# Optimization experiments

Hardware: AMD Instinct MI355X
Metric: run time of the kernel (lower is better)

## Reference

```python
import jax, jax.numpy as jnp
from jax import lax
import numpy as np

DIM = 64
NUM_HEADS = 1
HEAD_DIM = DIM // NUM_HEADS
SR = 8
EPS = 1e-5


def setup_inputs() -> dict:
    key = jax.random.key(0)
    ks = jax.random.split(key, 12)
    B, H, W = 8, 128, 128
    N = H * W
    s = 1.0 / np.sqrt(DIM)
    x = jax.random.normal(ks[0], (B, N, DIM), dtype=jnp.float32)
    Wq = jax.random.normal(ks[1], (DIM, DIM), dtype=jnp.float32) * s
    bq = jnp.zeros((DIM,), jnp.float32)
    Wk = jax.random.normal(ks[2], (DIM, DIM), dtype=jnp.float32) * s
    bk = jnp.zeros((DIM,), jnp.float32)
    Wv = jax.random.normal(ks[3], (DIM, DIM), dtype=jnp.float32) * s
    bv = jnp.zeros((DIM,), jnp.float32)
    # Conv2D kernel in HWIO layout (Keras default), kernel=stride=SR, padding VALID
    Wsr = jax.random.normal(ks[4], (SR, SR, DIM, DIM), dtype=jnp.float32) * (1.0 / np.sqrt(SR * SR * DIM))
    bsr = jnp.zeros((DIM,), jnp.float32)
    gamma = jnp.ones((DIM,), jnp.float32)
    beta = jnp.zeros((DIM,), jnp.float32)
    Wp = jax.random.normal(ks[5], (DIM, DIM), dtype=jnp.float32) * s
    bp = jnp.zeros((DIM,), jnp.float32)
    return {"x": x, "Wq": Wq, "bq": bq, "Wk": Wk, "bk": bk, "Wv": Wv, "bv": bv,
            "Wsr": Wsr, "bsr": bsr, "gamma": gamma, "beta": beta, "Wp": Wp, "bp": bp,
            "H": H, "W": W}


def reference(x, Wq, bq, Wk, bk, Wv, bv, Wsr, bsr, gamma, beta, Wp, bp, H, W):
    B, N, C = x.shape
    # queries: [B, heads, N, head_dim]
    q = (x @ Wq + bq).reshape(B, N, NUM_HEADS, HEAD_DIM).transpose(0, 2, 1, 3)
    # spatial reduction: strided conv over the token grid, then LayerNorm
    xs = x.reshape(B, H, W, C)
    xs = lax.conv_general_dilated(xs, Wsr, window_strides=(SR, SR), padding='VALID',
                                  dimension_numbers=('NHWC', 'HWIO', 'NHWC')) + bsr
    xs = xs.reshape(B, -1, C)  # [B, Nkv, C], Nkv = (H//SR)*(W//SR)
    mu = jnp.mean(xs, axis=-1, keepdims=True)
    var = jnp.var(xs, axis=-1, keepdims=True)
    xs = (xs - mu) * lax.rsqrt(var + EPS) * gamma + beta
    k = (xs @ Wk + bk).reshape(B, -1, NUM_HEADS, HEAD_DIM).transpose(0, 2, 1, 3)
    v = (xs @ Wv + bv).reshape(B, -1, NUM_HEADS, HEAD_DIM).transpose(0, 2, 1, 3)
    scale = jnp.asarray(np.sqrt(HEAD_DIM), x.dtype)
    attn = jnp.einsum('bhqd,bhkd->bhqk', q, k) / scale
    attn = jax.nn.softmax(attn, axis=-1)
    out = jnp.einsum('bhqk,bhkd->bhqd', attn, v)
    out = out.transpose(0, 2, 1, 3).reshape(B, N, NUM_HEADS * HEAD_DIM)
    return out @ Wp + bp
```

## Files before the change

kernel.cpp:

```cpp
#include <hip/hip_runtime.h>

typedef unsigned short u16;
typedef short short8 __attribute__((ext_vector_type(8)));
typedef short short4v __attribute__((ext_vector_type(4)));
typedef float f32x4 __attribute__((ext_vector_type(4)));
typedef float f4 __attribute__((ext_vector_type(4)));

#define MFMA16(a, b, c) __builtin_amdgcn_mfma_f32_16x16x32_bf16(a, b, c, 0, 0, 0)
#define MFMA1K(a, b, c) __builtin_amdgcn_mfma_f32_16x16x16bf16_1k(a, b, c, 0, 0, 0)

__device__ inline u16 f2bf(float f) {
    unsigned int v = __builtin_bit_cast(unsigned int, f);
    unsigned int r = (v + 0x7FFFu + ((v >> 16) & 1u)) >> 16;
    return (u16)r;
}
__device__ inline short4v pack4(f4 v) {
    short4v r;
#pragma unroll
    for (int j = 0; j < 4; ++j) r[j] = (short)f2bf(v[j]);
    return r;
}

__global__ __launch_bounds__(256) void prep_kernel(
    const float* __restrict__ Wsr, const float* __restrict__ Wq,
    const float* __restrict__ Wp,
    u16* __restrict__ WsrT, u16* __restrict__ WqT, u16* __restrict__ WpT)
{
    const int bid = blockIdx.x;
    const int tid = threadIdx.x;
    __shared__ float sT[64 * 65];
    const float* src;
    u16* dst;
    if (bid < 64)      { src = Wsr + (size_t)bid * 4096; dst = WsrT + (size_t)bid * 4096; }
    else if (bid == 64){ src = Wq;  dst = WqT; }
    else               { src = Wp;  dst = WpT; }
#pragma unroll
    for (int p = 0; p < 4; ++p) {
        int idx = p * 256 + tid;
        int r = idx >> 4, c4 = (idx & 15) * 4;
        f4 v = *(const f4*)(src + r * 64 + c4);
#pragma unroll
        for (int j = 0; j < 4; ++j) sT[r * 65 + c4 + j] = v[j];
    }
    __syncthreads();
#pragma unroll
    for (int p = 0; p < 2; ++p) {
        int idx = p * 256 + tid;
        int co = idx >> 3, g = (idx & 7) * 8;
        short8 o;
#pragma unroll
        for (int j = 0; j < 8; ++j) o[j] = (short)f2bf(sT[(g + j) * 65 + co]);
        *(short8*)(dst + (size_t)co * 64 + g) = o;
    }
}

__global__ __launch_bounds__(256) void conv_partial_kernel(
    const float* __restrict__ x, const u16* __restrict__ WsrT,
    float* __restrict__ partials)
{
    const int mtile  = blockIdx.x & 31;
    const int ksplit = blockIdx.x >> 5;
    const int tid  = threadIdx.x;
    const int wave = tid >> 6;
    const int lane = tid & 63;
    const int l15  = lane & 15;
    const int quad = lane >> 4;

    __shared__ u16 sA[64 * 72];
    __shared__ u16 sB[64 * 72];

    f32x4 acc[4];
#pragma unroll
    for (int nt = 0; nt < 4; ++nt) { acc[nt][0]=0.f; acc[nt][1]=0.f; acc[nt][2]=0.f; acc[nt][3]=0.f; }

    const int token0 = mtile * 64;
    for (int chunk = 0; chunk < 4; ++chunk) {
        const int cell = ksplit * 4 + chunk;
        const int py = cell >> 3, px = cell & 7;
        __syncthreads();
#pragma unroll
        for (int p = 0; p < 4; ++p) {
            int idx = p * 256 + tid;
            int r = idx >> 4, c4 = (idx & 15) * 4;
            int token = token0 + r;
            int b = token >> 8, rm = token & 255;
            int oy = rm >> 4, ox = rm & 15;
            int y = oy * 8 + py, xc = ox * 8 + px;
            f4 xv = *(const f4*)(x + ((size_t)(b * 16384 + y * 128 + xc)) * 64 + c4);
            short4v s;
#pragma unroll
            for (int j = 0; j < 4; ++j) s[j] = (short)f2bf(xv[j]);
            *(short4v*)&sA[r * 72 + c4] = s;
        }
#pragma unroll
        for (int p = 0; p < 2; ++p) {
            int idx = p * 256 + tid;
            int co = idx >> 3, g = (idx & 7) * 8;
            *(short8*)&sB[co * 72 + g] =
                *(const short8*)(WsrT + (size_t)cell * 4096 + co * 64 + g);
        }
        __syncthreads();
#pragma unroll
        for (int ks = 0; ks < 2; ++ks) {
            short8 af = *(const short8*)&sA[(wave * 16 + l15) * 72 + ks * 32 + quad * 8];
#pragma unroll
            for (int nt = 0; nt < 4; ++nt) {
                short8 bf = *(const short8*)&sB[(nt * 16 + l15) * 72 + ks * 32 + quad * 8];
                acc[nt] = MFMA16(af, bf, acc[nt]);
            }
        }
    }
    float* outp = partials + (size_t)ksplit * 131072;
#pragma unroll
    for (int nt = 0; nt < 4; ++nt)
#pragma unroll
        for (int i = 0; i < 4; ++i) {
            int row = token0 + wave * 16 + quad * 4 + i;
            outp[(size_t)row * 64 + nt * 16 + l15] = acc[nt][i];
        }
}

__global__ __launch_bounds__(256) void lnkv_kernel(
    const float* __restrict__ partials, const float* __restrict__ bsr,
    const float* __restrict__ gamma, const float* __restrict__ beta,
    const float* __restrict__ Wk, const float* __restrict__ bk,
    const float* __restrict__ Wv, const float* __restrict__ bv,
    u16* __restrict__ kbuf, u16* __restrict__ vTbuf)
{
    const int wave = threadIdx.x >> 6;
    const int c    = threadIdx.x & 63;
    const int token = blockIdx.x * 4 + wave;

    float acc = 0.f;
#pragma unroll
    for (int s = 0; s < 16; ++s)
        acc += partials[(size_t)s * 131072 + (size_t)token * 64 + c];
    acc += bsr[c];

    float sum = acc, sumsq = acc * acc;
#pragma unroll
    for (int m = 1; m < 64; m <<= 1) {
        sum   += __shfl_xor(sum, m, 64);
        sumsq += __shfl_xor(sumsq, m, 64);
    }
    float mean = sum * (1.f / 64.f);
    float var  = sumsq * (1.f / 64.f) - mean * mean;
    float inv  = rsqrtf(var + 1e-5f);
    float xn   = (acc - mean) * inv * gamma[c] + beta[c];

    __shared__ float sxn[4][64];
    sxn[wave][c] = xn;

    float ka = bk[c], va = bv[c];
#pragma unroll 8
    for (int ci = 0; ci < 64; ++ci) {
        float xv = sxn[wave][ci];
        ka += xv * Wk[ci * 64 + c];
        va += xv * Wv[ci * 64 + c];
    }
    kbuf[(size_t)token * 64 + c] = f2bf(ka);
    int b = token >> 8, t = token & 255;
    vTbuf[(size_t)b * 16384 + c * 256 + t] = f2bf(va);
}

__global__ __launch_bounds__(512) void attn_kernel(
    const float* __restrict__ x, const u16* __restrict__ WqT,
    const float* __restrict__ bq, const u16* __restrict__ WpT,
    const float* __restrict__ bp, const u16* __restrict__ kbuf,
    const u16* __restrict__ vTbuf, float* __restrict__ out)
{
    const int batch = blockIdx.x >> 6;
    const int row0  = (blockIdx.x & 63) * 256;
    const int tid  = threadIdx.x;
    const int wave = tid >> 6;
    const int lane = tid & 63;
    const int l15  = lane & 15;
    const int quad = lane >> 4;

    __shared__ u16 sK[256 * 72];
    __shared__ u16 sV[64 * 264];
    __shared__ u16 sWq[64 * 72];
    __shared__ u16 sWp[64 * 72];

#pragma unroll
    for (int p = 0; p < 4; ++p) {
        int idx = p * 512 + tid; int tt = idx >> 3, seg = idx & 7;
        *(short8*)&sK[tt * 72 + seg * 8] =
            *(const short8*)(kbuf + ((size_t)(batch * 256 + tt)) * 64 + seg * 8);
    }
#pragma unroll
    for (int p = 0; p < 4; ++p) {
        int idx = p * 512 + tid; int d = idx >> 5, seg = idx & 31;
        *(short8*)&sV[d * 264 + seg * 8] =
            *(const short8*)(vTbuf + ((size_t)(batch * 64 + d)) * 256 + seg * 8);
    }
    {
        int co = tid >> 3, g = (tid & 7) * 8;
        *(short8*)&sWq[co * 72 + g] = *(const short8*)(WqT + (size_t)co * 64 + g);
        *(short8*)&sWp[co * 72 + g] = *(const short8*)(WpT + (size_t)co * 64 + g);
    }
    __syncthreads();

    const int qbase = row0 + wave * 32;

    f32x4 qT[2][4];
#pragma unroll
    for (int qt = 0; qt < 2; ++qt)
#pragma unroll
        for (int ct = 0; ct < 4; ++ct) { qT[qt][ct][0]=0.f; qT[qt][ct][1]=0.f; qT[qt][ct][2]=0.f; qT[qt][ct][3]=0.f; }
#pragma unroll
    for (int kt = 0; kt < 4; ++kt) {
        short4v bfr[2];
#pragma unroll
        for (int qt = 0; qt < 2; ++qt) {
            f4 xv = *(const f4*)(x + ((size_t)(batch * 16384 + qbase + qt * 16 + l15)) * 64 + kt * 16 + quad * 4);
            bfr[qt] = pack4(xv);
        }
#pragma unroll
        for (int ct = 0; ct < 4; ++ct) {
            short4v a = *(const short4v*)&sWq[(ct * 16 + l15) * 72 + kt * 16 + quad * 4];
#pragma unroll
            for (int qt = 0; qt < 2; ++qt) qT[qt][ct] = MFMA1K(a, bfr[qt], qT[qt][ct]);
        }
    }
    short4v qf[2][4];
#pragma unroll
    for (int ct = 0; ct < 4; ++ct) {
        f4 bqv = *(const f4*)(bq + ct * 16 + quad * 4);
#pragma unroll
        for (int qt = 0; qt < 2; ++qt) {
            f4 t;
#pragma unroll
            for (int i = 0; i < 4; ++i) t[i] = (qT[qt][ct][i] + bqv[i]) * 0.125f;
            qf[qt][ct] = pack4(t);
        }
    }

    f32x4 st[2][16];
#pragma unroll
    for (int qt = 0; qt < 2; ++qt)
#pragma unroll
        for (int mt = 0; mt < 16; ++mt) { st[qt][mt][0]=0.f; st[qt][mt][1]=0.f; st[qt][mt][2]=0.f; st[qt][mt][3]=0.f; }
#pragma unroll
    for (int mt = 0; mt < 16; ++mt)
#pragma unroll
        for (int kt = 0; kt < 4; ++kt) {
            short4v a = *(const short4v*)&sK[(mt * 16 + l15) * 72 + kt * 16 + quad * 4];
#pragma unroll
            for (int qt = 0; qt < 2; ++qt) st[qt][mt] = MFMA1K(a, qf[qt][kt], st[qt][mt]);
        }

    short4v pf[2][16];
    float linv[2];
#pragma unroll
    for (int qt = 0; qt < 2; ++qt) {
        float mx = -1e30f;
#pragma unroll
        for (int mt = 0; mt < 16; ++mt)
#pragma unroll
            for (int i = 0; i < 4; ++i) mx = fmaxf(mx, st[qt][mt][i]);
        mx = fmaxf(mx, __shfl_xor(mx, 16, 64));
        mx = fmaxf(mx, __shfl_xor(mx, 32, 64));
        float l = 0.f;
#pragma unroll
        for (int mt = 0; mt < 16; ++mt) {
            f4 e;
#pragma unroll
            for (int i = 0; i < 4; ++i) { e[i] = __expf(st[qt][mt][i] - mx); l += e[i]; }
            pf[qt][mt] = pack4(e);
        }
        l += __shfl_xor(l, 16, 64);
        l += __shfl_xor(l, 32, 64);
        linv[qt] = 1.0f / l;
    }

    f32x4 ot[2][4];
#pragma unroll
    for (int qt = 0; qt < 2; ++qt)
#pragma unroll
        for (int dt = 0; dt < 4; ++dt) { ot[qt][dt][0]=0.f; ot[qt][dt][1]=0.f; ot[qt][dt][2]=0.f; ot[qt][dt][3]=0.f; }
#pragma unroll
    for (int mt = 0; mt < 16; ++mt)
#pragma unroll
        for (int dt = 0; dt < 4; ++dt) {
            short4v a = *(const short4v*)&sV[(dt * 16 + l15) * 264 + mt * 16 + quad * 4];
#pragma unroll
            for (int qt = 0; qt < 2; ++qt) ot[qt][dt] = MFMA1K(a, pf[qt][mt], ot[qt][dt]);
        }

    short4v of[2][4];
#pragma unroll
    for (int dt = 0; dt < 4; ++dt)
#pragma unroll
        for (int qt = 0; qt < 2; ++qt) {
            f4 t;
#pragma unroll
            for (int i = 0; i < 4; ++i) t[i] = ot[qt][dt][i] * linv[qt];
            of[qt][dt] = pack4(t);
        }
    f32x4 ft[2][4];
#pragma unroll
    for (int qt = 0; qt < 2; ++qt)
#pragma unroll
        for (int ct = 0; ct < 4; ++ct) { ft[qt][ct][0]=0.f; ft[qt][ct][1]=0.f; ft[qt][ct][2]=0.f; ft[qt][ct][3]=0.f; }
#pragma unroll
    for (int kt = 0; kt < 4; ++kt)
#pragma unroll
        for (int ct = 0; ct < 4; ++ct) {
            short4v a = *(const short4v*)&sWp[(ct * 16 + l15) * 72 + kt * 16 + quad * 4];
#pragma unroll
            for (int qt = 0; qt < 2; ++qt) ft[qt][ct] = MFMA1K(a, of[qt][kt], ft[qt][ct]);
        }

#pragma unroll
    for (int ct = 0; ct < 4; ++ct) {
        f4 bpv = *(const f4*)(bp + ct * 16 + quad * 4);
#pragma unroll
        for (int qt = 0; qt < 2; ++qt) {
            f4 r;
#pragma unroll
            for (int i = 0; i < 4; ++i) r[i] = ft[qt][ct][i] + bpv[i];
            *(f4*)(out + ((size_t)(batch * 16384 + qbase + qt * 16 + l15)) * 64 + ct * 16 + quad * 4) = r;
        }
    }
}

extern "C" void kernel_launch(void* const* d_in, const int* in_sizes, int n_in,
                              void* d_out, int out_size, void* d_ws, size_t ws_size,
                              hipStream_t stream) {
    const float* x     = (const float*)d_in[0];
    const float* Wq    = (const float*)d_in[1];
    const float* bq    = (const float*)d_in[2];
    const float* Wk    = (const float*)d_in[3];
    const float* bk    = (const float*)d_in[4];
    const float* Wv    = (const float*)d_in[5];
    const float* bv    = (const float*)d_in[6];
    const float* Wsr   = (const float*)d_in[7];
    const float* bsr   = (const float*)d_in[8];
    const float* gamma = (const float*)d_in[9];
    const float* beta  = (const float*)d_in[10];
    const float* Wp    = (const float*)d_in[11];
    const float* bp    = (const float*)d_in[12];

    char* w = (char*)d_ws;
    float* partials = (float*)w;
    u16* kbuf  = (u16*)(w + 8388608);
    u16* vTbuf = (u16*)(w + 8388608 + 262144);
    u16* WsrT  = (u16*)(w + 8388608 + 524288);
    u16* WqT   = (u16*)(w + 8388608 + 524288 + 524288);
    u16* WpT   = (u16*)(w + 8388608 + 524288 + 524288 + 8192);
    float* out = (float*)d_out;

    prep_kernel<<<66, 256, 0, stream>>>(Wsr, Wq, Wp, WsrT, WqT, WpT);
    conv_partial_kernel<<<512, 256, 0, stream>>>(x, WsrT, partials);
    lnkv_kernel<<<512, 256, 0, stream>>>(partials, bsr, gamma, beta, Wk, bk, Wv, bv, kbuf, vTbuf);
    attn_kernel<<<512, 512, 0, stream>>>(x, WqT, bq, WpT, bp, kbuf, vTbuf, out);
}
```

Before: 143.9 us.

## Fuse strided conv with LayerNorm and K/V projection, prefetch x in attention

Merges the split-K conv partial kernel and the LayerNorm+KV kernel into one kernel. Each block handles 8 tokens, and each wave accumulates 16 of the 64 kernel cells through MFMA reading directly from global memory. Partial sums are reduced in shared memory, which removes the 8 MB partials buffer round-trip and one launch. Half the MFMA rows are wasted, since only 8 tokens are padded into 16-row tiles, and only 256 blocks launch. The attention kernel also issues its x loads before the K/V shared-memory fill to hide their latency.

```diff
diff --git a/kernel.cpp b/kernel.cpp
--- a/kernel.cpp
+++ b/kernel.cpp
@@ -54,113 +54,91 @@
     }
 }
 
-__global__ __launch_bounds__(256) void conv_partial_kernel(
+__global__ __launch_bounds__(256) void convlnkv_kernel(
     const float* __restrict__ x, const u16* __restrict__ WsrT,
-    float* __restrict__ partials)
+    const float* __restrict__ bsr,
+    const float* __restrict__ gamma, const float* __restrict__ beta,
+    const float* __restrict__ Wk, const float* __restrict__ bk,
+    const float* __restrict__ Wv, const float* __restrict__ bv,
+    u16* __restrict__ kbuf, u16* __restrict__ vTbuf)
 {
-    const int mtile  = blockIdx.x & 31;
-    const int ksplit = blockIdx.x >> 5;
     const int tid  = threadIdx.x;
     const int wave = tid >> 6;
     const int lane = tid & 63;
     const int l15  = lane & 15;
     const int quad = lane >> 4;
 
-    __shared__ u16 sA[64 * 72];
-    __shared__ u16 sB[64 * 72];
+    const int t0   = blockIdx.x * 8;
+    const int bimg = t0 >> 8;
+    const int rm0  = t0 & 255;
+    const int oy   = rm0 >> 4;
+    const int ox   = (rm0 & 15) + (l15 & 7);
 
     f32x4 acc[4];
 #pragma unroll
     for (int nt = 0; nt < 4; ++nt) { acc[nt][0]=0.f; acc[nt][1]=0.f; acc[nt][2]=0.f; acc[nt][3]=0.f; }
 
-    const int token0 = mtile * 64;
-    for (int chunk = 0; chunk < 4; ++chunk) {
-        const int cell = ksplit * 4 + chunk;
+#pragma unroll
+    for (int i = 0; i < 16; ++i) {
+        const int cell = wave * 16 + i;
         const int py = cell >> 3, px = cell & 7;
-        __syncthreads();
-#pragma unroll
-        for (int p = 0; p < 4; ++p) {
-            int idx = p * 256 + tid;
-            int r = idx >> 4, c4 = (idx & 15) * 4;
-            int token = token0 + r;
-            int b = token >> 8, rm = token & 255;
-            int oy = rm >> 4, ox = rm & 15;
-            int y = oy * 8 + py, xc = ox * 8 + px;
-            f4 xv = *(const f4*)(x + ((size_t)(b * 16384 + y * 128 + xc)) * 64 + c4);
-            short4v s;
-#pragma unroll
-            for (int j = 0; j < 4; ++j) s[j] = (short)f2bf(xv[j]);
-            *(short4v*)&sA[r * 72 + c4] = s;
-        }
-#pragma unroll
-        for (int p = 0; p < 2; ++p) {
-            int idx = p * 256 + tid;
-            int co = idx >> 3, g = (idx & 7) * 8;
-            *(short8*)&sB[co * 72 + g] =
-                *(const short8*)(WsrT + (size_t)cell * 4096 + co * 64 + g);
-        }
-        __syncthreads();
+        const float* xp = x + ((size_t)(bimg * 16384 + (oy * 8 + py) * 128 + ox * 8 + px)) * 64;
+        const u16*   wp = WsrT + (size_t)cell * 4096;
 #pragma unroll
         for (int ks = 0; ks < 2; ++ks) {
-            short8 af = *(const short8*)&sA[(wave * 16 + l15) * 72 + ks * 32 + quad * 8];
+            f4 x0 = *(const f4*)(xp + ks * 32 + quad * 8);
+            f4 x1 = *(const f4*)(xp + ks * 32 + quad * 8 + 4);
+            short8 af;
+#pragma unroll
+            for (int j = 0; j < 4; ++j) { af[j] = (short)f2bf(x0[j]); af[4 + j] = (short)f2bf(x1[j]); }
 #pragma unroll
             for (int nt = 0; nt < 4; ++nt) {
-                short8 bf = *(const short8*)&sB[(nt * 16 + l15) * 72 + ks * 32 + quad * 8];
+                short8 bf = *(const short8*)(wp + (nt * 16 + l15) * 64 + ks * 32 + quad * 8);
                 acc[nt] = MFMA16(af, bf, acc[nt]);
             }
         }
     }
-    float* outp = partials + (size_t)ksplit * 131072;
-#pragma unroll
-    for (int nt = 0; nt < 4; ++nt)
-#pragma unroll
-        for (int i = 0; i < 4; ++i) {
-            int row = token0 + wave * 16 + quad * 4 + i;
-            outp[(size_t)row * 64 + nt * 16 + l15] = acc[nt][i];
-        }
-}
-
-__global__ __launch_bounds__(256) void lnkv_kernel(
-    const float* __restrict__ partials, const float* __restrict__ bsr,
-    const float* __restrict__ gamma, const float* __restrict__ beta,
-    const float* __restrict__ Wk, const float* __restrict__ bk,
-    const float* __restrict__ Wv, const float* __restrict__ bv,
-    u16* __restrict__ kbuf, u16* __restrict__ vTbuf)
-{
-    const int wave = threadIdx.x >> 6;
-    const int c    = threadIdx.x & 63;
-    const int token = blockIdx.x * 4 + wave;
-
-    float acc = 0.f;
-#pragma unroll
-    for (int s = 0; s < 16; ++s)
-        acc += partials[(size_t)s * 131072 + (size_t)token * 64 + c];
-    acc += bsr[c];
-
-    float sum = acc, sumsq = acc * acc;
-#pragma unroll
-    for (int m = 1; m < 64; m <<= 1) {
-        sum   += __shfl_xor(sum, m, 64);
-        sumsq += __shfl_xor(sumsq, m, 64);
-    }
-    float mean = sum * (1.f / 64.f);
-    float var  = sumsq * (1.f / 64.f) - mean * mean;
-    float inv  = rsqrtf(var + 1e-5f);
-    float xn   = (acc - mean) * inv * gamma[c] + beta[c];
-
-    __shared__ float sxn[4][64];
-    sxn[wave][c] = xn;
-
-    float ka = bk[c], va = bv[c];
+
+    __shared__ float red[4][8][64];
+    if (quad < 2) {
+#pragma unroll
+        for (int nt = 0; nt < 4; ++nt)
+#pragma unroll
+            for (int i = 0; i < 4; ++i)
+                red[wave][quad * 4 + i][nt * 16 + l15] = acc[nt][i];
+    }
+    __syncthreads();
+
+    __shared__ float sxn[8][64];
+#pragma unroll
+    for (int s = 0; s < 2; ++s) {
+        const int tt    = wave * 2 + s;
+        const int token = t0 + tt;
+        const int c     = lane;
+        float a = red[0][tt][c] + red[1][tt][c] + red[2][tt][c] + red[3][tt][c] + bsr[c];
+        float sum = a, sumsq = a * a;
+#pragma unroll
+        for (int m = 1; m < 64; m <<= 1) {
+            sum   += __shfl_xor(sum, m, 64);
+            sumsq += __shfl_xor(sumsq, m, 64);
+        }
+        float mean = sum * (1.f / 64.f);
+        float var  = sumsq * (1.f / 64.f) - mean * mean;
+        float inv  = rsqrtf(var + 1e-5f);
+        float xn   = (a - mean) * inv * gamma[c] + beta[c];
+        sxn[tt][c] = xn;
+
+        float ka = bk[c], va = bv[c];
 #pragma unroll 8
-    for (int ci = 0; ci < 64; ++ci) {
-        float xv = sxn[wave][ci];
-        ka += xv * Wk[ci * 64 + c];
-        va += xv * Wv[ci * 64 + c];
-    }
-    kbuf[(size_t)token * 64 + c] = f2bf(ka);
-    int b = token >> 8, t = token & 255;
-    vTbuf[(size_t)b * 16384 + c * 256 + t] = f2bf(va);
+        for (int ci = 0; ci < 64; ++ci) {
+            float xv = sxn[tt][ci];
+            ka += xv * Wk[ci * 64 + c];
+            va += xv * Wv[ci * 64 + c];
+        }
+        kbuf[(size_t)token * 64 + c] = f2bf(ka);
+        int bb = token >> 8, tloc = token & 255;
+        vTbuf[(size_t)bb * 16384 + c * 256 + tloc] = f2bf(va);
+    }
 }
 
 __global__ __launch_bounds__(512) void attn_kernel(
@@ -182,6 +160,15 @@
     __shared__ u16 sWq[64 * 72];
     __shared__ u16 sWp[64 * 72];
 
+    const int qbase = row0 + wave * 32;
+
+    f4 xq[4][2];
+#pragma unroll
+    for (int kt = 0; kt < 4; ++kt)
+#pragma unroll
+        for (int qt = 0; qt < 2; ++qt)
+            xq[kt][qt] = *(const f4*)(x + ((size_t)(batch * 16384 + qbase + qt * 16 + l15)) * 64 + kt * 16 + quad * 4);
+
 #pragma unroll
     for (int p = 0; p < 4; ++p) {
         int idx = p * 512 + tid; int tt = idx >> 3, seg = idx & 7;
@@ -201,8 +188,6 @@
     }
     __syncthreads();
 
-    const int qbase = row0 + wave * 32;
-
     f32x4 qT[2][4];
 #pragma unroll
     for (int qt = 0; qt < 2; ++qt)
@@ -212,10 +197,7 @@
     for (int kt = 0; kt < 4; ++kt) {
         short4v bfr[2];
 #pragma unroll
-        for (int qt = 0; qt < 2; ++qt) {
-            f4 xv = *(const f4*)(x + ((size_t)(batch * 16384 + qbase + qt * 16 + l15)) * 64 + kt * 16 + quad * 4);
-            bfr[qt] = pack4(xv);
-        }
+        for (int qt = 0; qt < 2; ++qt) bfr[qt] = pack4(xq[kt][qt]);
 #pragma unroll
         for (int ct = 0; ct < 4; ++ct) {
             short4v a = *(const short4v*)&sWq[(ct * 16 + l15) * 72 + kt * 16 + quad * 4];
@@ -343,16 +325,14 @@
     const float* bp    = (const float*)d_in[12];
 
     char* w = (char*)d_ws;
-    float* partials = (float*)w;
-    u16* kbuf  = (u16*)(w + 8388608);
-    u16* vTbuf = (u16*)(w + 8388608 + 262144);
-    u16* WsrT  = (u16*)(w + 8388608 + 524288);
-    u16* WqT   = (u16*)(w + 8388608 + 524288 + 524288);
-    u16* WpT   = (u16*)(w + 8388608 + 524288 + 524288 + 8192);
+    u16* kbuf  = (u16*)w;
+    u16* vTbuf = (u16*)(w + 262144);
+    u16* WsrT  = (u16*)(w + 524288);
+    u16* WqT   = (u16*)(w + 1048576);
+    u16* WpT   = (u16*)(w + 1048576 + 8192);
     float* out = (float*)d_out;
 
     prep_kernel<<<66, 256, 0, stream>>>(Wsr, Wq, Wp, WsrT, WqT, WpT);
-    conv_partial_kernel<<<512, 256, 0, stream>>>(x, WsrT, partials);
-    lnkv_kernel<<<512, 256, 0, stream>>>(partials, bsr, gamma, beta, Wk, bk, Wv, bv, kbuf, vTbuf);
+    convlnkv_kernel<<<256, 256, 0, stream>>>(x, WsrT, bsr, gamma, beta, Wk, bk, Wv, bv, kbuf, vTbuf);
     attn_kernel<<<512, 512, 0, stream>>>(x, WqT, bq, WpT, bp, kbuf, vTbuf, out);
 }
```

Result: slower. 156.5 us (+8.8%).

## Load conv operands directly from global into MFMA fragments; prefetch x in attention

Applied to the files above, without the earlier changes.

The conv partial kernel no longer stages the x tile and Wsr tile through shared memory. Each lane now loads its MFMA A fragment straight from global x, converts it to bf16, and reads B fragments directly from global WsrT, and the chunk loop is fully unrolled. This removes the shared-memory writes and two barriers per chunk, at the cost of less coalesced global loads and the same weight fragments being re-read from L1/L2 by every wave. In the attention kernel, the x rows for the Q projection are now issued into registers before the K/V/W shared-memory staging, so their latency overlaps that work, which raises register pressure.

```diff
diff --git a/kernel.cpp b/kernel.cpp
--- a/kernel.cpp
+++ b/kernel.cpp
@@ -66,46 +66,32 @@
     const int l15  = lane & 15;
     const int quad = lane >> 4;
 
-    __shared__ u16 sA[64 * 72];
-    __shared__ u16 sB[64 * 72];
-
     f32x4 acc[4];
 #pragma unroll
     for (int nt = 0; nt < 4; ++nt) { acc[nt][0]=0.f; acc[nt][1]=0.f; acc[nt][2]=0.f; acc[nt][3]=0.f; }
 
     const int token0 = mtile * 64;
+    const int token = token0 + wave * 16 + l15;
+    const int b  = token >> 8, rm = token & 255;
+    const int oy = rm >> 4,    ox = rm & 15;
+    const float* xbase = x + ((size_t)(b * 16384 + (oy * 8) * 128 + ox * 8)) * 64;
+
+#pragma unroll
     for (int chunk = 0; chunk < 4; ++chunk) {
         const int cell = ksplit * 4 + chunk;
         const int py = cell >> 3, px = cell & 7;
-        __syncthreads();
-#pragma unroll
-        for (int p = 0; p < 4; ++p) {
-            int idx = p * 256 + tid;
-            int r = idx >> 4, c4 = (idx & 15) * 4;
-            int token = token0 + r;
-            int b = token >> 8, rm = token & 255;
-            int oy = rm >> 4, ox = rm & 15;
-            int y = oy * 8 + py, xc = ox * 8 + px;
-            f4 xv = *(const f4*)(x + ((size_t)(b * 16384 + y * 128 + xc)) * 64 + c4);
-            short4v s;
-#pragma unroll
-            for (int j = 0; j < 4; ++j) s[j] = (short)f2bf(xv[j]);
-            *(short4v*)&sA[r * 72 + c4] = s;
-        }
-#pragma unroll
-        for (int p = 0; p < 2; ++p) {
-            int idx = p * 256 + tid;
-            int co = idx >> 3, g = (idx & 7) * 8;
-            *(short8*)&sB[co * 72 + g] =
-                *(const short8*)(WsrT + (size_t)cell * 4096 + co * 64 + g);
-        }
-        __syncthreads();
+        const float* xp = xbase + ((size_t)(py * 128 + px)) * 64;
+        const u16*   wp = WsrT + (size_t)cell * 4096;
 #pragma unroll
         for (int ks = 0; ks < 2; ++ks) {
-            short8 af = *(const short8*)&sA[(wave * 16 + l15) * 72 + ks * 32 + quad * 8];
+            f4 x0 = *(const f4*)(xp + ks * 32 + quad * 8);
+            f4 x1 = *(const f4*)(xp + ks * 32 + quad * 8 + 4);
+            short8 af;
+#pragma unroll
+            for (int j = 0; j < 4; ++j) { af[j] = (short)f2bf(x0[j]); af[4 + j] = (short)f2bf(x1[j]); }
 #pragma unroll
             for (int nt = 0; nt < 4; ++nt) {
-                short8 bf = *(const short8*)&sB[(nt * 16 + l15) * 72 + ks * 32 + quad * 8];
+                short8 bf = *(const short8*)(wp + (nt * 16 + l15) * 64 + ks * 32 + quad * 8);
                 acc[nt] = MFMA16(af, bf, acc[nt]);
             }
         }
@@ -182,6 +168,15 @@
     __shared__ u16 sWq[64 * 72];
     __shared__ u16 sWp[64 * 72];
 
+    const int qbase = row0 + wave * 32;
+
+    f4 xq[4][2];
+#pragma unroll
+    for (int kt = 0; kt < 4; ++kt)
+#pragma unroll
+        for (int qt = 0; qt < 2; ++qt)
+            xq[kt][qt] = *(const f4*)(x + ((size_t)(batch * 16384 + qbase + qt * 16 + l15)) * 64 + kt * 16 + quad * 4);
+
 #pragma unroll
     for (int p = 0; p < 4; ++p) {
         int idx = p * 512 + tid; int tt = idx >> 3, seg = idx & 7;
@@ -201,8 +196,6 @@
     }
     __syncthreads();
 
-    const int qbase = row0 + wave * 32;
-
     f32x4 qT[2][4];
 #pragma unroll
     for (int qt = 0; qt < 2; ++qt)
@@ -212,10 +205,7 @@
     for (int kt = 0; kt < 4; ++kt) {
         short4v bfr[2];
 #pragma unroll
-        for (int qt = 0; qt < 2; ++qt) {
-            f4 xv = *(const f4*)(x + ((size_t)(batch * 16384 + qbase + qt * 16 + l15)) * 64 + kt * 16 + quad * 4);
-            bfr[qt] = pack4(xv);
-        }
+        for (int qt = 0; qt < 2; ++qt) bfr[qt] = pack4(xq[kt][qt]);
 #pragma unroll
         for (int ct = 0; ct < 4; ++ct) {
             short4v a = *(const short4v*)&sWq[(ct * 16 + l15) * 72 + kt * 16 + quad * 4];
```

Result: slower. 150.3 us (+4.5%).

## Process query tiles sequentially to cut registers and raise attention occupancy

Applied to the files above, without the earlier changes.

The attention kernel now handles its two 16-row query tiles one after another in a loop instead of interleaved, which roughly halves the live accumulator and probability registers. Launch bounds request 4 blocks per CU. The Wq/Wp weights are read straight from global memory (cache) instead of being staged in LDS, which frees LDS and removes that staging step. The first tile's x rows are prefetched before the K/V LDS fill to overlap that load. The cost is less MFMA interleaving between independent tiles and repeated global weight reads per wave.

```diff
diff --git a/kernel.cpp b/kernel.cpp
--- a/kernel.cpp
+++ b/kernel.cpp
@@ -163,7 +163,7 @@
     vTbuf[(size_t)b * 16384 + c * 256 + t] = f2bf(va);
 }
 
-__global__ __launch_bounds__(512) void attn_kernel(
+__global__ __launch_bounds__(512, 4) void attn_kernel(
     const float* __restrict__ x, const u16* __restrict__ WqT,
     const float* __restrict__ bq, const u16* __restrict__ WpT,
     const float* __restrict__ bp, const u16* __restrict__ kbuf,
@@ -179,8 +179,13 @@
 
     __shared__ u16 sK[256 * 72];
     __shared__ u16 sV[64 * 264];
-    __shared__ u16 sWq[64 * 72];
-    __shared__ u16 sWp[64 * 72];
+
+    const int qbase = row0 + wave * 32;
+
+    f4 xq0[4];
+#pragma unroll
+    for (int kt = 0; kt < 4; ++kt)
+        xq0[kt] = *(const f4*)(x + ((size_t)(batch * 16384 + qbase + l15)) * 64 + kt * 16 + quad * 4);
 
 #pragma unroll
     for (int p = 0; p < 4; ++p) {
@@ -194,71 +199,60 @@
         *(short8*)&sV[d * 264 + seg * 8] =
             *(const short8*)(vTbuf + ((size_t)(batch * 64 + d)) * 256 + seg * 8);
     }
-    {
-        int co = tid >> 3, g = (tid & 7) * 8;
-        *(short8*)&sWq[co * 72 + g] = *(const short8*)(WqT + (size_t)co * 64 + g);
-        *(short8*)&sWp[co * 72 + g] = *(const short8*)(WpT + (size_t)co * 64 + g);
-    }
     __syncthreads();
 
-    const int qbase = row0 + wave * 32;
-
-    f32x4 qT[2][4];
-#pragma unroll
-    for (int qt = 0; qt < 2; ++qt)
-#pragma unroll
-        for (int ct = 0; ct < 4; ++ct) { qT[qt][ct][0]=0.f; qT[qt][ct][1]=0.f; qT[qt][ct][2]=0.f; qT[qt][ct][3]=0.f; }
-#pragma unroll
-    for (int kt = 0; kt < 4; ++kt) {
-        short4v bfr[2];
-#pragma unroll
-        for (int qt = 0; qt < 2; ++qt) {
-            f4 xv = *(const f4*)(x + ((size_t)(batch * 16384 + qbase + qt * 16 + l15)) * 64 + kt * 16 + quad * 4);
-            bfr[qt] = pack4(xv);
-        }
+    for (int qt = 0; qt < 2; ++qt) {
+        const int qrow = qbase + qt * 16 + l15;
+
+        f4 xq[4];
+        if (qt == 0) {
+#pragma unroll
+            for (int kt = 0; kt < 4; ++kt) xq[kt] = xq0[kt];
+        } else {
+#pragma unroll
+            for (int kt = 0; kt < 4; ++kt)
+                xq[kt] = *(const f4*)(x + ((size_t)(batch * 16384 + qrow)) * 64 + kt * 16 + quad * 4);
+        }
+
+        f32x4 qT[4];
+#pragma unroll
+        for (int ct = 0; ct < 4; ++ct) { qT[ct][0]=0.f; qT[ct][1]=0.f; qT[ct][2]=0.f; qT[ct][3]=0.f; }
+#pragma unroll
+        for (int kt = 0; kt < 4; ++kt) {
+            short4v bfr = pack4(xq[kt]);
+#pragma unroll
+            for (int ct = 0; ct < 4; ++ct) {
+                short4v a = *(const short4v*)(WqT + (size_t)(ct * 16 + l15) * 64 + kt * 16 + quad * 4);
+                qT[ct] = MFMA1K(a, bfr, qT[ct]);
+            }
+        }
+        short4v qf[4];
 #pragma unroll
         for (int ct = 0; ct < 4; ++ct) {
-            short4v a = *(const short4v*)&sWq[(ct * 16 + l15) * 72 + kt * 16 + quad * 4];
-#pragma unroll
-            for (int qt = 0; qt < 2; ++qt) qT[qt][ct] = MFMA1K(a, bfr[qt], qT[qt][ct]);
-        }
-    }
-    short4v qf[2][4];
-#pragma unroll
-    for (int ct = 0; ct < 4; ++ct) {
-        f4 bqv = *(const f4*)(bq + ct * 16 + quad * 4);
-#pragma unroll
-        for (int qt = 0; qt < 2; ++qt) {
+            f4 bqv = *(const f4*)(bq + ct * 16 + quad * 4);
             f4 t;
 #pragma unroll
-            for (int i = 0; i < 4; ++i) t[i] = (qT[qt][ct][i] + bqv[i]) * 0.125f;
-            qf[qt][ct] = pack4(t);
-        }
-    }
-
-    f32x4 st[2][16];
-#pragma unroll
-    for (int qt = 0; qt < 2; ++qt)
-#pragma unroll
-        for (int mt = 0; mt < 16; ++mt) { st[qt][mt][0]=0.f; st[qt][mt][1]=0.f; st[qt][mt][2]=0.f; st[qt][mt][3]=0.f; }
-#pragma unroll
-    for (int mt = 0; mt < 16; ++mt)
-#pragma unroll
-        for (int kt = 0; kt < 4; ++kt) {
-            short4v a = *(const short4v*)&sK[(mt * 16 + l15) * 72 + kt * 16 + quad * 4];
-#pragma unroll
-            for (int qt = 0; qt < 2; ++qt) st[qt][mt] = MFMA1K(a, qf[qt][kt], st[qt][mt]);
-        }
-
-    short4v pf[2][16];
-    float linv[2];
-#pragma unroll
-    for (int qt = 0; qt < 2; ++qt) {
+            for (int i = 0; i < 4; ++i) t[i] = (qT[ct][i] + bqv[i]) * 0.125f;
+            qf[ct] = pack4(t);
+        }
+
+        f32x4 st[16];
+#pragma unroll
+        for (int mt = 0; mt < 16; ++mt) { st[mt][0]=0.f; st[mt][1]=0.f; st[mt][2]=0.f; st[mt][3]=0.f; }
+#pragma unroll
+        for (int mt = 0; mt < 16; ++mt)
+#pragma unroll
+            for (int kt = 0; kt < 4; ++kt) {
+                short4v a = *(const short4v*)&sK[(mt * 16 + l15) * 72 + kt * 16 + quad * 4];
+                st[mt] = MFMA1K(a, qf[kt], st[mt]);
+            }
+
+        short4v pf[16];
         float mx = -1e30f;
 #pragma unroll
         for (int mt = 0; mt < 16; ++mt)
 #pragma unroll
-            for (int i = 0; i < 4; ++i) mx = fmaxf(mx, st[qt][mt][i]);
+            for (int i = 0; i < 4; ++i) mx = fmaxf(mx, st[mt][i]);
         mx = fmaxf(mx, __shfl_xor(mx, 16, 64));
         mx = fmaxf(mx, __shfl_xor(mx, 32, 64));
         float l = 0.f;
@@ -266,61 +260,50 @@
         for (int mt = 0; mt < 16; ++mt) {
             f4 e;
 #pragma unroll
-            for (int i = 0; i < 4; ++i) { e[i] = __expf(st[qt][mt][i] - mx); l += e[i]; }
-            pf[qt][mt] = pack4(e);
+            for (int i = 0; i < 4; ++i) { e[i] = __expf(st[mt][i] - mx); l += e[i]; }
+            pf[mt] = pack4(e);
         }
         l += __shfl_xor(l, 16, 64);
         l += __shfl_xor(l, 32, 64);
-        linv[qt] = 1.0f / l;
-    }
-
-    f32x4 ot[2][4];
-#pragma unroll
-    for (int qt = 0; qt < 2; ++qt)
-#pragma unroll
-        for (int dt = 0; dt < 4; ++dt) { ot[qt][dt][0]=0.f; ot[qt][dt][1]=0.f; ot[qt][dt][2]=0.f; ot[qt][dt][3]=0.f; }
-#pragma unroll
-    for (int mt = 0; mt < 16; ++mt)
+        const float linv = 1.0f / l;
+
+        f32x4 ot[4];
+#pragma unroll
+        for (int dt = 0; dt < 4; ++dt) { ot[dt][0]=0.f; ot[dt][1]=0.f; ot[dt][2]=0.f; ot[dt][3]=0.f; }
+#pragma unroll
+        for (int mt = 0; mt < 16; ++mt)
+#pragma unroll
+            for (int dt = 0; dt < 4; ++dt) {
+                short4v a = *(const short4v*)&sV[(dt * 16 + l15) * 264 + mt * 16 + quad * 4];
+                ot[dt] = MFMA1K(a, pf[mt], ot[dt]);
+            }
+
+        short4v of[4];
 #pragma unroll
         for (int dt = 0; dt < 4; ++dt) {
-            short4v a = *(const short4v*)&sV[(dt * 16 + l15) * 264 + mt * 16 + quad * 4];
-#pragma unroll
-            for (int qt = 0; qt < 2; ++qt) ot[qt][dt] = MFMA1K(a, pf[qt][mt], ot[qt][dt]);
-        }
-
-    short4v of[2][4];
-#pragma unroll
-    for (int dt = 0; dt < 4; ++dt)
-#pragma unroll
-        for (int qt = 0; qt < 2; ++qt) {
             f4 t;
 #pragma unroll
-            for (int i = 0; i < 4; ++i) t[i] = ot[qt][dt][i] * linv[qt];
-            of[qt][dt] = pack4(t);
-        }
-    f32x4 ft[2][4];
-#pragma unroll
-    for (int qt = 0; qt < 2; ++qt)
-#pragma unroll
-        for (int ct = 0; ct < 4; ++ct) { ft[qt][ct][0]=0.f; ft[qt][ct][1]=0.f; ft[qt][ct][2]=0.f; ft[qt][ct][3]=0.f; }
-#pragma unroll
-    for (int kt = 0; kt < 4; ++kt)
+            for (int i = 0; i < 4; ++i) t[i] = ot[dt][i] * linv;
+            of[dt] = pack4(t);
+        }
+        f32x4 ft[4];
+#pragma unroll
+        for (int ct = 0; ct < 4; ++ct) { ft[ct][0]=0.f; ft[ct][1]=0.f; ft[ct][2]=0.f; ft[ct][3]=0.f; }
+#pragma unroll
+        for (int kt = 0; kt < 4; ++kt)
+#pragma unroll
+            for (int ct = 0; ct < 4; ++ct) {
+                short4v a = *(const short4v*)(WpT + (size_t)(ct * 16 + l15) * 64 + kt * 16 + quad * 4);
+                ft[ct] = MFMA1K(a, of[kt], ft[ct]);
+            }
+
 #pragma unroll
         for (int ct = 0; ct < 4; ++ct) {
-            short4v a = *(const short4v*)&sWp[(ct * 16 + l15) * 72 + kt * 16 + quad * 4];
-#pragma unroll
-            for (int qt = 0; qt < 2; ++qt) ft[qt][ct] = MFMA1K(a, of[qt][kt], ft[qt][ct]);
-        }
-
-#pragma unroll
-    for (int ct = 0; ct < 4; ++ct) {
-        f4 bpv = *(const f4*)(bp + ct * 16 + quad * 4);
-#pragma unroll
-        for (int qt = 0; qt < 2; ++qt) {
+            f4 bpv = *(const f4*)(bp + ct * 16 + quad * 4);
             f4 r;
 #pragma unroll
-            for (int i = 0; i < 4; ++i) r[i] = ft[qt][ct][i] + bpv[i];
-            *(f4*)(out + ((size_t)(batch * 16384 + qbase + qt * 16 + l15)) * 64 + ct * 16 + quad * 4) = r;
+            for (int i = 0; i < 4; ++i) r[i] = ft[ct][i] + bpv[i];
+            *(f4*)(out + ((size_t)(batch * 16384 + qrow)) * 64 + ct * 16 + quad * 4) = r;
         }
     }
 }
```

Measured after the change: 373.2 us. 2.59x slower.
